# Kernel optimization log

Measured on AMD Instinct MI355X. Metric: run time of the kernel, lower is better.

## Reference

```python
import jax, jax.numpy as jnp
import numpy as np

SEQ, B, DIM, UNITS = 256, 64, 1024, 1024


def setup_inputs() -> dict:
    key = jax.random.key(0)
    k1, k2, k3, k4, k5, k6 = jax.random.split(key, 6)
    s = 1.0 / np.sqrt(UNITS)
    x = jax.random.normal(k1, (SEQ, B, DIM), dtype=jnp.float32)
    hx = jnp.zeros((B, UNITS), dtype=jnp.float32)
    cx = jnp.zeros((B, UNITS), dtype=jnp.float32)
    reset = (jax.random.uniform(k2, (SEQ, B, 1)) < 0.05).astype(jnp.float32)
    W_ih = jax.random.uniform(k3, (4 * UNITS, DIM), minval=-s, maxval=s, dtype=jnp.float32)
    W_hh = jax.random.uniform(k4, (4 * UNITS, UNITS), minval=-s, maxval=s, dtype=jnp.float32)
    b_ih = jax.random.uniform(k5, (4 * UNITS,), minval=-s, maxval=s, dtype=jnp.float32)
    b_hh = jax.random.uniform(k6, (4 * UNITS,), minval=-s, maxval=s, dtype=jnp.float32)
    return {"x": x, "hx": hx, "cx": cx, "reset": reset,
            "W_ih": W_ih, "W_hh": W_hh, "b_ih": b_ih, "b_hh": b_hh}


def _lstm_scan(x, hx, cx, mask, W_ih, W_hh, b_ih, b_hh):
    # Precompute input projections for all timesteps in one big GEMM:
    # [seq, b, dim] @ [dim, 4u] -> [seq, b, 4u]
    x_proj = jnp.einsum('sbd,gd->sbg', x, W_ih) + b_ih + b_hh

    def step(carry, inp):
        h, c = carry
        xp_t, m_t = inp               # xp_t: [b, 4u], m_t: [b, 1]
        h = h * m_t                   # reset hidden/cell state at episode starts
        c = c * m_t
        gates = xp_t + h @ W_hh.T     # [b, 4u]
        i, f, g, o = jnp.split(gates, 4, axis=-1)  # torch LSTMCell gate order
        i = jax.nn.sigmoid(i)
        f = jax.nn.sigmoid(f)
        g = jnp.tanh(g)
        o = jax.nn.sigmoid(o)
        c = f * c + i * g
        h = o * jnp.tanh(c)
        return (h, c), (h, c)

    (_, _), (hs, cs) = jax.lax.scan(step, (hx, cx), (x_proj, mask))
    return hs, cs  # each [seq, b, units]


def reference(x, hx, cx, reset, W_ih, W_hh, b_ih, b_hh):
    mask = 1.0 - reset  # [seq, b, 1]
    hs, cs = _lstm_scan(x, hx, cx, mask, W_ih, W_hh, b_ih, b_hh)
    # original returns (stacked outputs, per-step (h, c) states)
    return hs, hs, cs
```

## Files before the change

kernel.cpp:

```cpp
#include <hip/hip_runtime.h>
#include <stdint.h>

typedef unsigned short ushort_t;
typedef __attribute__((ext_vector_type(8))) short s16x8;
typedef __attribute__((ext_vector_type(4))) float f32x4;
typedef __attribute__((ext_vector_type(4))) unsigned short u16x4;

#define TO_GLB(p) ((const __attribute__((address_space(1))) void*)(p))
#define TO_LDS(p) ((__attribute__((address_space(3))) void*)(p))

__device__ __forceinline__ ushort_t f2bf(float f) {
  union { float f; uint32_t u; } v; v.f = f;
  uint32_t u = v.u;
  uint32_t r = (u + 0x7FFFu + ((u >> 16) & 1u)) >> 16;
  return (ushort_t)r;
}
__device__ __forceinline__ float bf2f(ushort_t b) {
  union { uint32_t u; float f; } v; v.u = ((uint32_t)b) << 16;
  return v.f;
}
__device__ __forceinline__ float sigm(float x) {
  x = fminf(fmaxf(x, -30.f), 30.f);
  return 1.0f / (1.0f + __expf(-x));
}
__device__ __forceinline__ float tanh_f(float x) {
  x = fminf(fmaxf(x, -15.f), 15.f);
  float t = __expf(2.0f * x);
  return (t - 1.0f) / (t + 1.0f);
}

__global__ void conv_f32_to_bf16(const float* __restrict__ src,
                                 ushort_t* __restrict__ dst, int n4) {
  int i = blockIdx.x * blockDim.x + threadIdx.x;
  if (i < n4) {
    float4 v = ((const float4*)src)[i];
    u16x4 o;
    o[0] = f2bf(v.x); o[1] = f2bf(v.y); o[2] = f2bf(v.z); o[3] = f2bf(v.w);
    *(u16x4*)(dst + 4 * (size_t)i) = o;
  }
}

__global__ void init_h(const float* __restrict__ hx, ushort_t* __restrict__ h0, int n) {
  int i = blockIdx.x * blockDim.x + threadIdx.x;
  if (i < n) h0[i] = f2bf(hx[i]);
}

__global__ __launch_bounds__(256) void gemm_xproj(
    const ushort_t* __restrict__ A,
    const ushort_t* __restrict__ Bw,
    const float* __restrict__ b_ih, const float* __restrict__ b_hh,
    ushort_t* __restrict__ C)
{
  __shared__ ushort_t As[128 * 32];
  __shared__ ushort_t Bs[128 * 32];
  const int t = threadIdx.x;
  const int lane = t & 63;
  const int wid = t >> 6;
  const int wr = wid >> 1, wc = wid & 1;
  const size_t tm = (size_t)blockIdx.x * 128;
  const size_t tn = (size_t)blockIdx.y * 128;

  f32x4 acc[4][4];
  const f32x4 zero = {0.f, 0.f, 0.f, 0.f};
#pragma unroll
  for (int m = 0; m < 4; m++)
#pragma unroll
    for (int n = 0; n < 4; n++) acc[m][n] = zero;

  for (int k0 = 0; k0 < 1024; k0 += 32) {
    __syncthreads();
#pragma unroll
    for (int i = 0; i < 2; i++) {
      int row = i * 64 + (t >> 2);
      int kc = (t & 3) * 8;
      const ushort_t* ga = A + (tm + row) * 1024 + k0 + kc;
      __builtin_amdgcn_global_load_lds(TO_GLB(ga),
          TO_LDS((char*)As + (i * 256 + wid * 64) * 16), 16, 0, 0);
      const ushort_t* gb = Bw + (tn + row) * 1024 + k0 + kc;
      __builtin_amdgcn_global_load_lds(TO_GLB(gb),
          TO_LDS((char*)Bs + (i * 256 + wid * 64) * 16), 16, 0, 0);
    }
    __syncthreads();
    s16x8 af[4], bfr[4];
#pragma unroll
    for (int m = 0; m < 4; m++) {
      int r = wr * 64 + m * 16 + (lane & 15);
      af[m] = *(const s16x8*)((const char*)As + r * 64 + (lane >> 4) * 16);
    }
#pragma unroll
    for (int n = 0; n < 4; n++) {
      int r = wc * 64 + n * 16 + (lane & 15);
      bfr[n] = *(const s16x8*)((const char*)Bs + r * 64 + (lane >> 4) * 16);
    }
#pragma unroll
    for (int m = 0; m < 4; m++)
#pragma unroll
      for (int n = 0; n < 4; n++)
        acc[m][n] = __builtin_amdgcn_mfma_f32_16x16x32_bf16(af[m], bfr[n], acc[m][n], 0, 0, 0);
  }

#pragma unroll
  for (int m = 0; m < 4; m++)
#pragma unroll
    for (int n = 0; n < 4; n++)
#pragma unroll
      for (int j = 0; j < 4; j++) {
        size_t row = tm + wr * 64 + m * 16 + ((lane >> 4) << 2) + j;
        int col = (int)tn + wc * 64 + n * 16 + (lane & 15);
        float v = acc[m][n][j] + b_ih[col] + b_hh[col];
        C[row * 4096 + col] = f2bf(v);
      }
}

__global__ __launch_bounds__(512, 2) void lstm_scan(
    const ushort_t* __restrict__ whhb,
    const ushort_t* __restrict__ xproj,
    const float* __restrict__ reset,
    const float* __restrict__ cx,
    ushort_t* __restrict__ h0buf, ushort_t* __restrict__ h1buf,
    unsigned int* __restrict__ flags,
    float* __restrict__ out_h0, float* __restrict__ out_h1,
    float* __restrict__ out_cs)
{
  __shared__ char smem[43520];
  char* hs = smem;
  float* gsh = (float*)(smem + 32768);

  const int t = threadIdx.x;
  const int lane = t & 63;
  const int w = t >> 6;
  const int ns = w & 3;
  const int kh = w >> 2;
  const int j16 = lane & 15;
  const int q = lane >> 4;
  const int blk = blockIdx.x;
  const int bg = blk >> 6;
  const int ug = blk & 63;
  const int b0 = bg * 16;
  const int u0 = ug * 16;

  s16x8 bfrag[16];
  {
    const ushort_t* wrow = whhb + ((size_t)(ns * 1024 + u0 + j16)) * 1024 + kh * 512 + q * 8;
#pragma unroll
    for (int kk = 0; kk < 16; kk++)
      bfrag[kk] = *(const s16x8*)(wrow + kk * 32);
  }
#pragma unroll
  for (int kk = 0; kk < 16; kk++)
    asm volatile("" : "+v"(bfrag[kk]));

  const int b_local = t >> 4;
  const int lu = t & 15;
  const bool upd = (t < 256);
  float c_reg = 0.0f;
  if (upd) c_reg = cx[(size_t)(b0 + b_local) * 1024 + u0 + lu];

  const int sr = t & 15;
  const int sc = t >> 4;
  const int swz = (sr & 7) << 4;
  const s16x8 zv = {0, 0, 0, 0, 0, 0, 0, 0};
  const f32x4 fzero = {0.f, 0.f, 0.f, 0.f};

  for (int s = 0; s < 256; s++) {
    const ushort_t* hc = (s & 1) ? h1buf : h0buf;
    ushort_t* hn = (s & 1) ? h0buf : h1buf;

    float xv0 = 0.f, xv1 = 0.f, xv2 = 0.f, xv3 = 0.f, m2 = 0.f;
    if (upd) {
      const ushort_t* xpp = xproj + ((size_t)s * 64 + b0 + b_local) * 4096 + u0 + lu;
      xv0 = bf2f(xpp[0]);
      xv1 = bf2f(xpp[1024]);
      xv2 = bf2f(xpp[2048]);
      xv3 = bf2f(xpp[3072]);
      m2 = 1.0f - reset[s * 64 + b0 + b_local];
    }
    float mrow = reset[s * 64 + b0 + sr];

    if (s > 0) {
      const unsigned int* fp = flags + bg * 64 + lane;
      while (__hip_atomic_load(fp, __ATOMIC_RELAXED, __HIP_MEMORY_SCOPE_AGENT)
             < (unsigned int)s) {}
      asm volatile("" ::: "memory");
    }

    {
      const char* srcp = (const char*)(hc + (size_t)(b0 + sr) * 1024 + sc * 32);
      s16x8 v0, v1, v2, v3;
      asm volatile("global_load_dwordx4 %0, %1, off sc0 sc1" : "=v"(v0) : "v"(srcp));
      asm volatile("global_load_dwordx4 %0, %1, off offset:16 sc0 sc1" : "=v"(v1) : "v"(srcp));
      asm volatile("global_load_dwordx4 %0, %1, off offset:32 sc0 sc1" : "=v"(v2) : "v"(srcp));
      asm volatile("global_load_dwordx4 %0, %1, off offset:48 sc0 sc1" : "=v"(v3) : "v"(srcp));
      asm volatile("s_waitcnt vmcnt(0)" ::: "memory");
      __builtin_amdgcn_sched_barrier(0);
      if (mrow != 0.0f) { v0 = zv; v1 = zv; v2 = zv; v3 = zv; }
      const int base = sr * 2048 + sc * 64;
      *(s16x8*)(hs + ((base + 0)  ^ swz)) = v0;
      *(s16x8*)(hs + ((base + 16) ^ swz)) = v1;
      *(s16x8*)(hs + ((base + 32) ^ swz)) = v2;
      *(s16x8*)(hs + ((base + 48) ^ swz)) = v3;
    }
    __syncthreads();

    f32x4 acc = fzero;
#pragma unroll
    for (int kk = 0; kk < 16; kk++) {
      int off = (j16 * 2048 + kh * 1024 + kk * 64 + q * 16) ^ ((j16 & 7) << 4);
      s16x8 a = *(const s16x8*)(hs + off);
      acc = __builtin_amdgcn_mfma_f32_16x16x32_bf16(a, bfrag[kk], acc, 0, 0, 0);
    }
#pragma unroll
    for (int kk = 0; kk < 16; kk++)
      asm volatile("" : "+v"(bfrag[kk]));

#pragma unroll
    for (int jj = 0; jj < 4; jj++)
      gsh[kh * 1344 + (q * 4 + jj) * 84 + ns * 16 + j16] = acc[jj];
    __syncthreads();

    float hv = 0.0f, cn = 0.0f;
    if (upd) {
      const float* g0p = gsh + b_local * 84;
      const float* g1p = gsh + 1344 + b_local * 84;
      float gv0 = g0p[lu]      + g1p[lu]      + xv0;
      float gv1 = g0p[16 + lu] + g1p[16 + lu] + xv1;
      float gv2 = g0p[32 + lu] + g1p[32 + lu] + xv2;
      float gv3 = g0p[48 + lu] + g1p[48 + lu] + xv3;
      float ii = sigm(gv0), ff = sigm(gv1), G = tanh_f(gv2), oo = sigm(gv3);
      cn = ff * (c_reg * m2) + ii * G;
      hv = oo * tanh_f(cn);
      c_reg = cn;

      unsigned int mybits = (unsigned int)f2bf(hv);
      unsigned int pb = (unsigned int)__shfl_xor((int)mybits, 1, 64);
      if ((t & 1) == 0) {
        unsigned int pack = mybits | (pb << 16);
        __hip_atomic_store(
            (unsigned int*)(hn + (size_t)(b0 + b_local) * 1024 + u0 + lu),
            pack, __ATOMIC_RELAXED, __HIP_MEMORY_SCOPE_AGENT);
      }
    }

    asm volatile("s_waitcnt vmcnt(0)" ::: "memory");
    __syncthreads();
    if (t == 0)
      __hip_atomic_store(&flags[blk], (unsigned int)(s + 1),
                         __ATOMIC_RELAXED, __HIP_MEMORY_SCOPE_AGENT);

    if (upd) {
      size_t ob = ((size_t)s * 64 + b0 + b_local) * 1024 + u0 + lu;
      out_cs[ob] = cn;
      out_h0[ob] = hv;
      out_h1[ob] = hv;
    }
  }
}

extern "C" void kernel_launch(void* const* d_in, const int* in_sizes, int n_in,
                              void* d_out, int out_size, void* d_ws, size_t ws_size,
                              hipStream_t stream) {
  const float* x     = (const float*)d_in[0];
  const float* hx    = (const float*)d_in[1];
  const float* cx    = (const float*)d_in[2];
  const float* reset = (const float*)d_in[3];
  const float* W_ih  = (const float*)d_in[4];
  const float* W_hh  = (const float*)d_in[5];
  const float* b_ih  = (const float*)d_in[6];
  const float* b_hh  = (const float*)d_in[7];
  float* out = (float*)d_out;

  char* ws = (char*)d_ws;
  ushort_t* xbf   = (ushort_t*)(ws);
  ushort_t* wihb  = (ushort_t*)(ws + 33554432);
  ushort_t* whhb  = (ushort_t*)(ws + 41943040);
  ushort_t* xproj = (ushort_t*)(ws + 50331648);
  ushort_t* h0    = (ushort_t*)(ws + 184549376);
  ushort_t* h1    = (ushort_t*)(ws + 184680448);
  unsigned int* flags = (unsigned int*)(ws + 184811520);

  hipMemsetAsync(flags, 0, 256 * sizeof(unsigned int), stream);
  hipLaunchKernelGGL(conv_f32_to_bf16, dim3(16384), dim3(256), 0, stream, x, xbf, 4194304);
  hipLaunchKernelGGL(conv_f32_to_bf16, dim3(4096), dim3(256), 0, stream, W_ih, wihb, 1048576);
  hipLaunchKernelGGL(conv_f32_to_bf16, dim3(4096), dim3(256), 0, stream, W_hh, whhb, 1048576);
  hipLaunchKernelGGL(init_h, dim3(256), dim3(256), 0, stream, hx, h0, 65536);
  hipLaunchKernelGGL(gemm_xproj, dim3(128, 32), dim3(256), 0, stream, xbf, wihb, b_ih, b_hh, xproj);

  float* oh0 = out;
  float* oh1 = out + 16777216;
  float* ocs = out + 33554432;

  const ushort_t* whhb_c = whhb;
  const ushort_t* xproj_c = xproj;
  void* args[] = {(void*)&whhb_c, (void*)&xproj_c, (void*)&reset, (void*)&cx,
                  (void*)&h0, (void*)&h1, (void*)&flags,
                  (void*)&oh0, (void*)&oh1, (void*)&ocs};
  hipLaunchCooperativeKernel((void*)lstm_scan, dim3(256), dim3(512), args, 0, stream);
}
```

Measured before the change: 1.518 ms.

## Replace flag-based step barrier with sentinel-filled per-step hidden-state history polling

Drops the per-block flag array and the spin on flags before each step. Every timestep now writes h into its own slot of a full sequence buffer that was pre-filled with 0xFFFF sentinels, and consumers poll the data itself until no sentinel remains. This removes the trailing vmcnt wait, the extra __syncthreads and the flag store, and it skips loading h for rows that are reset. In exchange it adds a fill kernel over a 32MB buffer, which reuses the xbf workspace. It also relies on a valid bf16 h never being 0xFFFF, which is a NaN pattern, and on the 32-bit packed stores being seen atomically.

```diff
diff --git a/kernel.cpp b/kernel.cpp
--- a/kernel.cpp
+++ b/kernel.cpp
@@ -5,6 +5,7 @@
 typedef __attribute__((ext_vector_type(8))) short s16x8;
 typedef __attribute__((ext_vector_type(4))) float f32x4;
 typedef __attribute__((ext_vector_type(4))) unsigned short u16x4;
+typedef __attribute__((ext_vector_type(4))) unsigned int u32x4;
 
 #define TO_GLB(p) ((const __attribute__((address_space(1))) void*)(p))
 #define TO_LDS(p) ((__attribute__((address_space(3))) void*)(p))
@@ -37,6 +38,14 @@
     u16x4 o;
     o[0] = f2bf(v.x); o[1] = f2bf(v.y); o[2] = f2bf(v.z); o[3] = f2bf(v.w);
     *(u16x4*)(dst + 4 * (size_t)i) = o;
+  }
+}
+
+__global__ void fill_sentinel(unsigned int* __restrict__ dst, int n16) {
+  int i = blockIdx.x * blockDim.x + threadIdx.x;
+  if (i < n16) {
+    u32x4 v = {0xFFFFFFFFu, 0xFFFFFFFFu, 0xFFFFFFFFu, 0xFFFFFFFFu};
+    *(u32x4*)(dst + 4 * (size_t)i) = v;
   }
 }
 
@@ -117,8 +126,7 @@
     const ushort_t* __restrict__ xproj,
     const float* __restrict__ reset,
     const float* __restrict__ cx,
-    ushort_t* __restrict__ h0buf, ushort_t* __restrict__ h1buf,
-    unsigned int* __restrict__ flags,
+    ushort_t* __restrict__ hseq,
     float* __restrict__ out_h0, float* __restrict__ out_h1,
     float* __restrict__ out_cs)
 {
@@ -163,8 +171,8 @@
   const f32x4 fzero = {0.f, 0.f, 0.f, 0.f};
 
   for (int s = 0; s < 256; s++) {
-    const ushort_t* hc = (s & 1) ? h1buf : h0buf;
-    ushort_t* hn = (s & 1) ? h0buf : h1buf;
+    const char* hc = (const char*)hseq + (size_t)s * 131072;
+    ushort_t* hn = hseq + (size_t)(s + 1) * 65536;
 
     float xv0 = 0.f, xv1 = 0.f, xv2 = 0.f, xv3 = 0.f, m2 = 0.f;
     if (upd) {
@@ -177,23 +185,28 @@
     }
     float mrow = reset[s * 64 + b0 + sr];
 
-    if (s > 0) {
-      const unsigned int* fp = flags + bg * 64 + lane;
-      while (__hip_atomic_load(fp, __ATOMIC_RELAXED, __HIP_MEMORY_SCOPE_AGENT)
-             < (unsigned int)s) {}
-      asm volatile("" ::: "memory");
-    }
-
+    s16x8 v0 = zv, v1 = zv, v2 = zv, v3 = zv;
+    if (mrow == 0.0f) {
+      const char* srcp = hc + (size_t)(b0 + sr) * 2048 + sc * 64;
+      int clean;
+      do {
+        asm volatile("global_load_dwordx4 %0, %1, off sc0 sc1" : "=v"(v0) : "v"(srcp));
+        asm volatile("global_load_dwordx4 %0, %1, off offset:16 sc0 sc1" : "=v"(v1) : "v"(srcp));
+        asm volatile("global_load_dwordx4 %0, %1, off offset:32 sc0 sc1" : "=v"(v2) : "v"(srcp));
+        asm volatile("global_load_dwordx4 %0, %1, off offset:48 sc0 sc1" : "=v"(v3) : "v"(srcp));
+        asm volatile("s_waitcnt vmcnt(0)" ::: "memory");
+        clean = 1;
+#pragma unroll
+        for (int i = 0; i < 8; i++) {
+          clean &= (v0[i] != (short)-1);
+          clean &= (v1[i] != (short)-1);
+          clean &= (v2[i] != (short)-1);
+          clean &= (v3[i] != (short)-1);
+        }
+      } while (!clean);
+    }
+    __builtin_amdgcn_sched_barrier(0);
     {
-      const char* srcp = (const char*)(hc + (size_t)(b0 + sr) * 1024 + sc * 32);
-      s16x8 v0, v1, v2, v3;
-      asm volatile("global_load_dwordx4 %0, %1, off sc0 sc1" : "=v"(v0) : "v"(srcp));
-      asm volatile("global_load_dwordx4 %0, %1, off offset:16 sc0 sc1" : "=v"(v1) : "v"(srcp));
-      asm volatile("global_load_dwordx4 %0, %1, off offset:32 sc0 sc1" : "=v"(v2) : "v"(srcp));
-      asm volatile("global_load_dwordx4 %0, %1, off offset:48 sc0 sc1" : "=v"(v3) : "v"(srcp));
-      asm volatile("s_waitcnt vmcnt(0)" ::: "memory");
-      __builtin_amdgcn_sched_barrier(0);
-      if (mrow != 0.0f) { v0 = zv; v1 = zv; v2 = zv; v3 = zv; }
       const int base = sr * 2048 + sc * 64;
       *(s16x8*)(hs + ((base + 0)  ^ swz)) = v0;
       *(s16x8*)(hs + ((base + 16) ^ swz)) = v1;
@@ -218,7 +231,6 @@
       gsh[kh * 1344 + (q * 4 + jj) * 84 + ns * 16 + j16] = acc[jj];
     __syncthreads();
 
-    float hv = 0.0f, cn = 0.0f;
     if (upd) {
       const float* g0p = gsh + b_local * 84;
       const float* g1p = gsh + 1344 + b_local * 84;
@@ -227,8 +239,8 @@
       float gv2 = g0p[32 + lu] + g1p[32 + lu] + xv2;
       float gv3 = g0p[48 + lu] + g1p[48 + lu] + xv3;
       float ii = sigm(gv0), ff = sigm(gv1), G = tanh_f(gv2), oo = sigm(gv3);
-      cn = ff * (c_reg * m2) + ii * G;
-      hv = oo * tanh_f(cn);
+      float cn = ff * (c_reg * m2) + ii * G;
+      float hv = oo * tanh_f(cn);
       c_reg = cn;
 
       unsigned int mybits = (unsigned int)f2bf(hv);
@@ -239,15 +251,7 @@
             (unsigned int*)(hn + (size_t)(b0 + b_local) * 1024 + u0 + lu),
             pack, __ATOMIC_RELAXED, __HIP_MEMORY_SCOPE_AGENT);
       }
-    }
-
-    asm volatile("s_waitcnt vmcnt(0)" ::: "memory");
-    __syncthreads();
-    if (t == 0)
-      __hip_atomic_store(&flags[blk], (unsigned int)(s + 1),
-                         __ATOMIC_RELAXED, __HIP_MEMORY_SCOPE_AGENT);
-
-    if (upd) {
+
       size_t ob = ((size_t)s * 64 + b0 + b_local) * 1024 + u0 + lu;
       out_cs[ob] = cn;
       out_h0[ob] = hv;
@@ -274,16 +278,16 @@
   ushort_t* wihb  = (ushort_t*)(ws + 33554432);
   ushort_t* whhb  = (ushort_t*)(ws + 41943040);
   ushort_t* xproj = (ushort_t*)(ws + 50331648);
-  ushort_t* h0    = (ushort_t*)(ws + 184549376);
-  ushort_t* h1    = (ushort_t*)(ws + 184680448);
-  unsigned int* flags = (unsigned int*)(ws + 184811520);
-
-  hipMemsetAsync(flags, 0, 256 * sizeof(unsigned int), stream);
+  ushort_t* hseq  = (ushort_t*)(ws);
+
   hipLaunchKernelGGL(conv_f32_to_bf16, dim3(16384), dim3(256), 0, stream, x, xbf, 4194304);
   hipLaunchKernelGGL(conv_f32_to_bf16, dim3(4096), dim3(256), 0, stream, W_ih, wihb, 1048576);
   hipLaunchKernelGGL(conv_f32_to_bf16, dim3(4096), dim3(256), 0, stream, W_hh, whhb, 1048576);
-  hipLaunchKernelGGL(init_h, dim3(256), dim3(256), 0, stream, hx, h0, 65536);
   hipLaunchKernelGGL(gemm_xproj, dim3(128, 32), dim3(256), 0, stream, xbf, wihb, b_ih, b_hh, xproj);
+
+  hipLaunchKernelGGL(fill_sentinel, dim3(8192), dim3(256), 0, stream,
+                     (unsigned int*)(hseq + 65536), 2097152);
+  hipLaunchKernelGGL(init_h, dim3(256), dim3(256), 0, stream, hx, hseq, 65536);
 
   float* oh0 = out;
   float* oh1 = out + 16777216;
@@ -292,7 +296,6 @@
   const ushort_t* whhb_c = whhb;
   const ushort_t* xproj_c = xproj;
   void* args[] = {(void*)&whhb_c, (void*)&xproj_c, (void*)&reset, (void*)&cx,
-                  (void*)&h0, (void*)&h1, (void*)&flags,
-                  (void*)&oh0, (void*)&oh1, (void*)&ocs};
+                  (void*)&hseq, (void*)&oh0, (void*)&oh1, (void*)&ocs};
   hipLaunchCooperativeKernel((void*)lstm_scan, dim3(256), dim3(512), args, 0, stream);
 }
```

After: 1.775 ms. 16.9% more time.

## Use per-wave fine-grained flags and skip polling for reset rows

Applied to the files above, without the earlier changes.

Replaces the single per-block step flag with per-wave flags, one for each group of 4 batch rows, so each update wave publishes its flag once its own h stores drain, with no block-wide barrier. Consumers poll only the two producer flags (one 64-bit load) covering the row and column slice they read, rather than all 64 blocks in the group. Rows whose reset flag is set skip both the polling and the h load, since their state is zeroed anyway. This cuts barrier and polling latency on the serial recurrence, at the cost of a larger flag array and more complex ordering between waves.

```diff
diff --git a/kernel.cpp b/kernel.cpp
--- a/kernel.cpp
+++ b/kernel.cpp
@@ -118,7 +118,7 @@
     const float* __restrict__ reset,
     const float* __restrict__ cx,
     ushort_t* __restrict__ h0buf, ushort_t* __restrict__ h1buf,
-    unsigned int* __restrict__ flags,
+    unsigned int* __restrict__ flags3,
     float* __restrict__ out_h0, float* __restrict__ out_h1,
     float* __restrict__ out_cs)
 {
@@ -162,6 +162,10 @@
   const s16x8 zv = {0, 0, 0, 0, 0, 0, 0, 0};
   const f32x4 fzero = {0.f, 0.f, 0.f, 0.f};
 
+  const unsigned long long* pollp = (const unsigned long long*)
+      (flags3 + ((bg * 4 + (sr >> 2)) * 64 + 2 * sc));
+  unsigned int* myflag = flags3 + ((bg * 4 + w) * 64 + ug);
+
   for (int s = 0; s < 256; s++) {
     const ushort_t* hc = (s & 1) ? h1buf : h0buf;
     ushort_t* hn = (s & 1) ? h0buf : h1buf;
@@ -177,23 +181,26 @@
     }
     float mrow = reset[s * 64 + b0 + sr];
 
-    if (s > 0) {
-      const unsigned int* fp = flags + bg * 64 + lane;
-      while (__hip_atomic_load(fp, __ATOMIC_RELAXED, __HIP_MEMORY_SCOPE_AGENT)
-             < (unsigned int)s) {}
-      asm volatile("" ::: "memory");
-    }
+    if (s > 0 && mrow == 0.0f) {
+      unsigned long long pv;
+      do {
+        pv = __hip_atomic_load(pollp, __ATOMIC_RELAXED, __HIP_MEMORY_SCOPE_AGENT);
+      } while ((unsigned int)pv < (unsigned int)s ||
+               (unsigned int)(pv >> 32) < (unsigned int)s);
+    }
+    asm volatile("" ::: "memory");
 
     {
-      const char* srcp = (const char*)(hc + (size_t)(b0 + sr) * 1024 + sc * 32);
-      s16x8 v0, v1, v2, v3;
-      asm volatile("global_load_dwordx4 %0, %1, off sc0 sc1" : "=v"(v0) : "v"(srcp));
-      asm volatile("global_load_dwordx4 %0, %1, off offset:16 sc0 sc1" : "=v"(v1) : "v"(srcp));
-      asm volatile("global_load_dwordx4 %0, %1, off offset:32 sc0 sc1" : "=v"(v2) : "v"(srcp));
-      asm volatile("global_load_dwordx4 %0, %1, off offset:48 sc0 sc1" : "=v"(v3) : "v"(srcp));
-      asm volatile("s_waitcnt vmcnt(0)" ::: "memory");
+      s16x8 v0 = zv, v1 = zv, v2 = zv, v3 = zv;
+      if (mrow == 0.0f) {
+        const char* srcp = (const char*)(hc + (size_t)(b0 + sr) * 1024 + sc * 32);
+        asm volatile("global_load_dwordx4 %0, %1, off sc0 sc1" : "=v"(v0) : "v"(srcp));
+        asm volatile("global_load_dwordx4 %0, %1, off offset:16 sc0 sc1" : "=v"(v1) : "v"(srcp));
+        asm volatile("global_load_dwordx4 %0, %1, off offset:32 sc0 sc1" : "=v"(v2) : "v"(srcp));
+        asm volatile("global_load_dwordx4 %0, %1, off offset:48 sc0 sc1" : "=v"(v3) : "v"(srcp));
+        asm volatile("s_waitcnt vmcnt(0)" ::: "memory");
+      }
       __builtin_amdgcn_sched_barrier(0);
-      if (mrow != 0.0f) { v0 = zv; v1 = zv; v2 = zv; v3 = zv; }
       const int base = sr * 2048 + sc * 64;
       *(s16x8*)(hs + ((base + 0)  ^ swz)) = v0;
       *(s16x8*)(hs + ((base + 16) ^ swz)) = v1;
@@ -218,7 +225,6 @@
       gsh[kh * 1344 + (q * 4 + jj) * 84 + ns * 16 + j16] = acc[jj];
     __syncthreads();
 
-    float hv = 0.0f, cn = 0.0f;
     if (upd) {
       const float* g0p = gsh + b_local * 84;
       const float* g1p = gsh + 1344 + b_local * 84;
@@ -227,8 +233,8 @@
       float gv2 = g0p[32 + lu] + g1p[32 + lu] + xv2;
       float gv3 = g0p[48 + lu] + g1p[48 + lu] + xv3;
       float ii = sigm(gv0), ff = sigm(gv1), G = tanh_f(gv2), oo = sigm(gv3);
-      cn = ff * (c_reg * m2) + ii * G;
-      hv = oo * tanh_f(cn);
+      float cn = ff * (c_reg * m2) + ii * G;
+      float hv = oo * tanh_f(cn);
       c_reg = cn;
 
       unsigned int mybits = (unsigned int)f2bf(hv);
@@ -236,18 +242,15 @@
       if ((t & 1) == 0) {
         unsigned int pack = mybits | (pb << 16);
         __hip_atomic_store(
-            (unsigned int*)(hn + (size_t)(b0 + b_local) * 1024 + u0 + lu),
+            (unsigned int*)(hn + (size_t)(b_local + b0) * 1024 + u0 + lu),
             pack, __ATOMIC_RELAXED, __HIP_MEMORY_SCOPE_AGENT);
       }
-    }
-
-    asm volatile("s_waitcnt vmcnt(0)" ::: "memory");
-    __syncthreads();
-    if (t == 0)
-      __hip_atomic_store(&flags[blk], (unsigned int)(s + 1),
-                         __ATOMIC_RELAXED, __HIP_MEMORY_SCOPE_AGENT);
-
-    if (upd) {
+
+      asm volatile("s_waitcnt vmcnt(0)" ::: "memory");
+      if (lane == 0)
+        __hip_atomic_store(myflag, (unsigned int)(s + 1),
+                           __ATOMIC_RELAXED, __HIP_MEMORY_SCOPE_AGENT);
+
       size_t ob = ((size_t)s * 64 + b0 + b_local) * 1024 + u0 + lu;
       out_cs[ob] = cn;
       out_h0[ob] = hv;
@@ -276,9 +279,9 @@
   ushort_t* xproj = (ushort_t*)(ws + 50331648);
   ushort_t* h0    = (ushort_t*)(ws + 184549376);
   ushort_t* h1    = (ushort_t*)(ws + 184680448);
-  unsigned int* flags = (unsigned int*)(ws + 184811520);
-
-  hipMemsetAsync(flags, 0, 256 * sizeof(unsigned int), stream);
+  unsigned int* flags3 = (unsigned int*)(ws + 184811520);
+
+  hipMemsetAsync(flags3, 0, 4096, stream);
   hipLaunchKernelGGL(conv_f32_to_bf16, dim3(16384), dim3(256), 0, stream, x, xbf, 4194304);
   hipLaunchKernelGGL(conv_f32_to_bf16, dim3(4096), dim3(256), 0, stream, W_ih, wihb, 1048576);
   hipLaunchKernelGGL(conv_f32_to_bf16, dim3(4096), dim3(256), 0, stream, W_hh, whhb, 1048576);
@@ -292,7 +295,7 @@
   const ushort_t* whhb_c = whhb;
   const ushort_t* xproj_c = xproj;
   void* args[] = {(void*)&whhb_c, (void*)&xproj_c, (void*)&reset, (void*)&cx,
-                  (void*)&h0, (void*)&h1, (void*)&flags,
+                  (void*)&h0, (void*)&h1, (void*)&flags3,
                   (void*)&oh0, (void*)&oh1, (void*)&ocs};
   hipLaunchCooperativeKernel((void*)lstm_scan, dim3(256), dim3(512), args, 0, stream);
 }
```

After: 1.808 ms. 1.19x slower.

## Fuse input projection GEMM into recurrent scan kernel with lookahead ring buffer

Applied to the files above, without the earlier changes.

Drops the separate x-projection GEMM kernel and its bf16 intermediate buffer. Instead, waves 4-7 of each scan block compute that block's slice of x@W_ih^T plus bias three timesteps ahead and store it in an LDS ring buffer, which the gate update then reads in place of global memory. This removes a large GEMM launch and its round trip through global memory, and uses idle waves during the serial recurrence. The cost is extra per-step MFMA work and W_ih/x loads on the recurrence critical path, plus more LDS per block, which may hurt occupancy or step latency.

```diff
diff --git a/kernel.cpp b/kernel.cpp
--- a/kernel.cpp
+++ b/kernel.cpp
@@ -45,86 +45,22 @@
   if (i < n) h0[i] = f2bf(hx[i]);
 }
 
-__global__ __launch_bounds__(256) void gemm_xproj(
-    const ushort_t* __restrict__ A,
-    const ushort_t* __restrict__ Bw,
-    const float* __restrict__ b_ih, const float* __restrict__ b_hh,
-    ushort_t* __restrict__ C)
-{
-  __shared__ ushort_t As[128 * 32];
-  __shared__ ushort_t Bs[128 * 32];
-  const int t = threadIdx.x;
-  const int lane = t & 63;
-  const int wid = t >> 6;
-  const int wr = wid >> 1, wc = wid & 1;
-  const size_t tm = (size_t)blockIdx.x * 128;
-  const size_t tn = (size_t)blockIdx.y * 128;
-
-  f32x4 acc[4][4];
-  const f32x4 zero = {0.f, 0.f, 0.f, 0.f};
-#pragma unroll
-  for (int m = 0; m < 4; m++)
-#pragma unroll
-    for (int n = 0; n < 4; n++) acc[m][n] = zero;
-
-  for (int k0 = 0; k0 < 1024; k0 += 32) {
-    __syncthreads();
-#pragma unroll
-    for (int i = 0; i < 2; i++) {
-      int row = i * 64 + (t >> 2);
-      int kc = (t & 3) * 8;
-      const ushort_t* ga = A + (tm + row) * 1024 + k0 + kc;
-      __builtin_amdgcn_global_load_lds(TO_GLB(ga),
-          TO_LDS((char*)As + (i * 256 + wid * 64) * 16), 16, 0, 0);
-      const ushort_t* gb = Bw + (tn + row) * 1024 + k0 + kc;
-      __builtin_amdgcn_global_load_lds(TO_GLB(gb),
-          TO_LDS((char*)Bs + (i * 256 + wid * 64) * 16), 16, 0, 0);
-    }
-    __syncthreads();
-    s16x8 af[4], bfr[4];
-#pragma unroll
-    for (int m = 0; m < 4; m++) {
-      int r = wr * 64 + m * 16 + (lane & 15);
-      af[m] = *(const s16x8*)((const char*)As + r * 64 + (lane >> 4) * 16);
-    }
-#pragma unroll
-    for (int n = 0; n < 4; n++) {
-      int r = wc * 64 + n * 16 + (lane & 15);
-      bfr[n] = *(const s16x8*)((const char*)Bs + r * 64 + (lane >> 4) * 16);
-    }
-#pragma unroll
-    for (int m = 0; m < 4; m++)
-#pragma unroll
-      for (int n = 0; n < 4; n++)
-        acc[m][n] = __builtin_amdgcn_mfma_f32_16x16x32_bf16(af[m], bfr[n], acc[m][n], 0, 0, 0);
-  }
-
-#pragma unroll
-  for (int m = 0; m < 4; m++)
-#pragma unroll
-    for (int n = 0; n < 4; n++)
-#pragma unroll
-      for (int j = 0; j < 4; j++) {
-        size_t row = tm + wr * 64 + m * 16 + ((lane >> 4) << 2) + j;
-        int col = (int)tn + wc * 64 + n * 16 + (lane & 15);
-        float v = acc[m][n][j] + b_ih[col] + b_hh[col];
-        C[row * 4096 + col] = f2bf(v);
-      }
-}
-
 __global__ __launch_bounds__(512, 2) void lstm_scan(
     const ushort_t* __restrict__ whhb,
-    const ushort_t* __restrict__ xproj,
+    const ushort_t* __restrict__ xbf,
+    const ushort_t* __restrict__ wihb,
+    const float* __restrict__ b_ih, const float* __restrict__ b_hh,
     const float* __restrict__ reset,
-    const float* __restrict__ cx,
+    const float* __restrict__ cxp,
     ushort_t* __restrict__ h0buf, ushort_t* __restrict__ h1buf,
     unsigned int* __restrict__ flags,
     float* __restrict__ out_h0, float* __restrict__ out_h1,
     float* __restrict__ out_cs)
 {
-  __shared__ char smem[43520];
+  __shared__ char smem[59904];
   char* hs = smem;
   float* gsh = (float*)(smem + 32768);
+  float* ring = (float*)(smem + 43520);
 
   const int t = threadIdx.x;
   const int lane = t & 63;
@@ -154,27 +90,44 @@
   const int lu = t & 15;
   const bool upd = (t < 256);
   float c_reg = 0.0f;
-  if (upd) c_reg = cx[(size_t)(b0 + b_local) * 1024 + u0 + lu];
+  if (upd) c_reg = cxp[(size_t)(b0 + b_local) * 1024 + u0 + lu];
+
+  const bool xw = (w >= 4);
+  const int xc_col = (w - 4) * 16 + j16;
+  const int wrow_i = ((xc_col & 3) << 10) + u0 + (xc_col >> 2);
+  const ushort_t* wih_p = wihb + (size_t)wrow_i * 1024 + q * 8;
+  float biasv = 0.0f;
+  if (xw) biasv = b_ih[wrow_i] + b_hh[wrow_i];
+
+  const f32x4 fzero = {0.f, 0.f, 0.f, 0.f};
+  auto do_xproj = [&](int T) {
+    f32x4 ax = fzero;
+    const ushort_t* xrow = xbf + ((size_t)T * 64 + b0 + j16) * 1024 + q * 8;
+#pragma unroll 8
+    for (int kk = 0; kk < 32; kk++) {
+      s16x8 a = *(const s16x8*)(xrow + kk * 32);
+      s16x8 bw = *(const s16x8*)(wih_p + kk * 32);
+      ax = __builtin_amdgcn_mfma_f32_16x16x32_bf16(a, bw, ax, 0, 0, 0);
+    }
+    float* rp = ring + (size_t)((T & 3) * 16) * 64 + xc_col;
+#pragma unroll
+    for (int r = 0; r < 4; r++)
+      rp[(q * 4 + r) * 64] = ax[r] + biasv;
+  };
+
+  if (xw) { do_xproj(0); do_xproj(1); do_xproj(2); }
 
   const int sr = t & 15;
   const int sc = t >> 4;
   const int swz = (sr & 7) << 4;
   const s16x8 zv = {0, 0, 0, 0, 0, 0, 0, 0};
-  const f32x4 fzero = {0.f, 0.f, 0.f, 0.f};
 
   for (int s = 0; s < 256; s++) {
     const ushort_t* hc = (s & 1) ? h1buf : h0buf;
     ushort_t* hn = (s & 1) ? h0buf : h1buf;
 
-    float xv0 = 0.f, xv1 = 0.f, xv2 = 0.f, xv3 = 0.f, m2 = 0.f;
-    if (upd) {
-      const ushort_t* xpp = xproj + ((size_t)s * 64 + b0 + b_local) * 4096 + u0 + lu;
-      xv0 = bf2f(xpp[0]);
-      xv1 = bf2f(xpp[1024]);
-      xv2 = bf2f(xpp[2048]);
-      xv3 = bf2f(xpp[3072]);
-      m2 = 1.0f - reset[s * 64 + b0 + b_local];
-    }
+    float m2 = 0.0f;
+    if (upd) m2 = 1.0f - reset[s * 64 + b0 + b_local];
     float mrow = reset[s * 64 + b0 + sr];
 
     if (s > 0) {
@@ -222,10 +175,11 @@
     if (upd) {
       const float* g0p = gsh + b_local * 84;
       const float* g1p = gsh + 1344 + b_local * 84;
-      float gv0 = g0p[lu]      + g1p[lu]      + xv0;
-      float gv1 = g0p[16 + lu] + g1p[16 + lu] + xv1;
-      float gv2 = g0p[32 + lu] + g1p[32 + lu] + xv2;
-      float gv3 = g0p[48 + lu] + g1p[48 + lu] + xv3;
+      f32x4 rv = *(const f32x4*)(ring + (size_t)((s & 3) * 16 + b_local) * 64 + lu * 4);
+      float gv0 = g0p[lu]      + g1p[lu]      + rv[0];
+      float gv1 = g0p[16 + lu] + g1p[16 + lu] + rv[1];
+      float gv2 = g0p[32 + lu] + g1p[32 + lu] + rv[2];
+      float gv3 = g0p[48 + lu] + g1p[48 + lu] + rv[3];
       float ii = sigm(gv0), ff = sigm(gv1), G = tanh_f(gv2), oo = sigm(gv3);
       cn = ff * (c_reg * m2) + ii * G;
       hv = oo * tanh_f(cn);
@@ -236,7 +190,7 @@
       if ((t & 1) == 0) {
         unsigned int pack = mybits | (pb << 16);
         __hip_atomic_store(
-            (unsigned int*)(hn + (size_t)(b0 + b_local) * 1024 + u0 + lu),
+            (unsigned int*)(hn + (size_t)(b_local + b0) * 1024 + u0 + lu),
             pack, __ATOMIC_RELAXED, __HIP_MEMORY_SCOPE_AGENT);
       }
     }
@@ -253,6 +207,7 @@
       out_h0[ob] = hv;
       out_h1[ob] = hv;
     }
+    if (xw && (s + 3 < 256)) do_xproj(s + 3);
   }
 }
 
@@ -273,25 +228,25 @@
   ushort_t* xbf   = (ushort_t*)(ws);
   ushort_t* wihb  = (ushort_t*)(ws + 33554432);
   ushort_t* whhb  = (ushort_t*)(ws + 41943040);
-  ushort_t* xproj = (ushort_t*)(ws + 50331648);
-  ushort_t* h0    = (ushort_t*)(ws + 184549376);
-  ushort_t* h1    = (ushort_t*)(ws + 184680448);
-  unsigned int* flags = (unsigned int*)(ws + 184811520);
-
-  hipMemsetAsync(flags, 0, 256 * sizeof(unsigned int), stream);
+  ushort_t* h0    = (ushort_t*)(ws + 50331648);
+  ushort_t* h1    = (ushort_t*)(ws + 50462720);
+  unsigned int* flags = (unsigned int*)(ws + 50593792);
+
+  hipMemsetAsync(flags, 0, 1024, stream);
   hipLaunchKernelGGL(conv_f32_to_bf16, dim3(16384), dim3(256), 0, stream, x, xbf, 4194304);
   hipLaunchKernelGGL(conv_f32_to_bf16, dim3(4096), dim3(256), 0, stream, W_ih, wihb, 1048576);
   hipLaunchKernelGGL(conv_f32_to_bf16, dim3(4096), dim3(256), 0, stream, W_hh, whhb, 1048576);
   hipLaunchKernelGGL(init_h, dim3(256), dim3(256), 0, stream, hx, h0, 65536);
-  hipLaunchKernelGGL(gemm_xproj, dim3(128, 32), dim3(256), 0, stream, xbf, wihb, b_ih, b_hh, xproj);
 
   float* oh0 = out;
   float* oh1 = out + 16777216;
   float* ocs = out + 33554432;
 
   const ushort_t* whhb_c = whhb;
-  const ushort_t* xproj_c = xproj;
-  void* args[] = {(void*)&whhb_c, (void*)&xproj_c, (void*)&reset, (void*)&cx,
+  const ushort_t* xbf_c = xbf;
+  const ushort_t* wihb_c = wihb;
+  void* args[] = {(void*)&whhb_c, (void*)&xbf_c, (void*)&wihb_c,
+                  (void*)&b_ih, (void*)&b_hh, (void*)&reset, (void*)&cx,
                   (void*)&h0, (void*)&h1, (void*)&flags,
                   (void*)&oh0, (void*)&oh1, (void*)&ocs};
   hipLaunchCooperativeKernel((void*)lstm_scan, dim3(256), dim3(512), args, 0, stream);
```

After: 2.694 ms. 77.4% more time.
